# Optimization experiments

Measured on AMD Instinct MI355X. Metric: run time of the kernel, lower is better.

Reference implementation:

```python
import jax, jax.numpy as jnp
import numpy as np

DT_SCALE = 0.01  # time grid = arange(T) * 0.01, i.e. t in [0, 0.99]


def setup_inputs() -> dict:
    key = jax.random.key(0)
    k1, k2, k3 = jax.random.split(key, 3)
    latents, hidden = 128, 256
    S, N, T = 4, 1024, 100
    first_point = jax.random.normal(k1, (S, N, latents), dtype=jnp.float32)
    time_steps_to_predict = jnp.arange(T, dtype=jnp.float32) * DT_SCALE
    # ODEFunc MLP params (Glorot-ish scaling so tanh stays in a sane range)
    W1 = jax.random.normal(k2, (latents, hidden), dtype=jnp.float32) / np.sqrt(latents)
    b1 = jnp.zeros((hidden,), dtype=jnp.float32)
    W2 = jax.random.normal(k3, (hidden, latents), dtype=jnp.float32) / np.sqrt(hidden)
    b2 = jnp.zeros((latents,), dtype=jnp.float32)
    return {
        "first_point": first_point,
        "time_steps_to_predict": time_steps_to_predict,
        "W1": W1, "b1": b1, "W2": W2, "b2": b2,
    }


def reference(first_point, time_steps_to_predict, W1, b1, W2, b2):
    # ode_func: dy/dt = tanh(y @ W1 + b1) @ W2 + b2 (time-autonomous MLP)
    def f(y):
        return jnp.tanh(y @ W1 + b1) @ W2 + b2

    # torchdiffeq fixed-step 'rk4': one classical RK4 step per output interval.
    t0s = time_steps_to_predict[:-1]
    t1s = time_steps_to_predict[1:]

    def rk4_step(y, ts):
        t0, t1 = ts
        dt = t1 - t0
        half = dt * 0.5
        k1 = f(y)
        k2 = f(y + half * k1)
        k3 = f(y + half * k2)
        k4 = f(y + dt * k3)
        y1 = y + (dt / 6.0) * (k1 + 2.0 * k2 + 2.0 * k3 + k4)
        return y1, y1

    _, ys = jax.lax.scan(rk4_step, first_point, (t0s, t1s))  # [T-1, S, N, D]
    pred_y = jnp.concatenate([first_point[None], ys], axis=0)  # [T, S, N, D]
    # permute(1, 2, 0, 3): [T, S, N, D] -> [S, N, T, D]
    return jnp.transpose(pred_y, (1, 2, 0, 3))
```

## Files before the change

### kernel.cpp

```cpp
#include <hip/hip_runtime.h>
#include <hip/hip_bf16.h>

typedef __attribute__((ext_vector_type(8))) short v8s;
typedef __attribute__((ext_vector_type(4))) float f4;

#define MFMA16(a, b, c) __builtin_amdgcn_mfma_f32_16x16x32_bf16((a), (b), (c), 0, 0, 0)

__device__ __forceinline__ float bf2f(unsigned short u) {
    return __uint_as_float(((unsigned)u) << 16);
}
__device__ __forceinline__ unsigned short f2bf(float x) {
    unsigned u = __float_as_uint(x);
    unsigned r = 0x7FFFu + ((u >> 16) & 1u);
    return (unsigned short)((u + r) >> 16);
}
__device__ __forceinline__ unsigned pack_bf16_2(float a, float b) {
    float2 t; t.x = a; t.y = b;
    union { __hip_bfloat162 h; unsigned u; } cv;
    cv.h = __float22bfloat162_rn(t);
    return cv.u;
}
__device__ __forceinline__ float tanh_fast(float z) {
    float u = __builtin_amdgcn_exp2f(z * 2.885390081777927f);
    float r = __builtin_amdgcn_rcpf(u + 1.0f);
    return __builtin_fmaf(-2.0f, r, 1.0f);
}
__device__ __forceinline__ float ldin(const void* p, int i, bool f32) {
    return f32 ? ((const float*)p)[i] : bf2f(((const unsigned short*)p)[i]);
}

#define BROWS 16
#define TSTEPS 100
#define DLAT 128
#define DHID 256
#define YSTR 136
#define HSTR 264

__global__ __launch_bounds__(512, 2)
void ode_rk4_kernel(const void* __restrict__ fp,
                    const void* __restrict__ ts,
                    const void* __restrict__ W1,
                    const void* __restrict__ b1,
                    const void* __restrict__ W2,
                    const void* __restrict__ b2,
                    void* __restrict__ out) {
    __shared__ unsigned short yB[BROWS * YSTR];
    __shared__ unsigned short hB[BROWS * HSTR];
    __shared__ float tsL[TSTEPS];

    const bool m32 = fabsf(((const float*)ts)[1] - 0.01f) < 0.004f;

    const int tid = threadIdx.x;
    const int w = tid >> 6;
    const int lane = tid & 63;
    const int pp = lane & 15;
    const int qq = lane >> 4;
    const int R0 = blockIdx.x * BROWS;

    if (tid < TSTEPS) tsL[tid] = ldin(ts, tid, m32);

    v8s w1f[4][2];
#pragma unroll
    for (int kt = 0; kt < 4; ++kt)
#pragma unroll
        for (int nt = 0; nt < 2; ++nt) {
            v8s f;
#pragma unroll
            for (int j = 0; j < 8; ++j)
                f[j] = (short)f2bf(ldin(W1, (kt * 32 + qq * 8 + j) * DHID + 32 * w + nt * 16 + pp, m32));
            w1f[kt][nt] = f;
        }
    v8s w2f[8];
#pragma unroll
    for (int kt = 0; kt < 8; ++kt) {
        v8s f;
#pragma unroll
        for (int j = 0; j < 8; ++j)
            f[j] = (short)f2bf(ldin(W2, (kt * 32 + qq * 8 + j) * DLAT + 16 * w + pp, m32));
        w2f[kt] = f;
    }
    const float b1v0 = ldin(b1, 32 * w + pp, m32);
    const float b1v1 = ldin(b1, 32 * w + 16 + pp, m32);
    const float b2v  = ldin(b2, 16 * w + pp, m32);

    const int pb = pp >> 3, pw = pp & 7;
    const int sA = (pp >> 1) & 7;
    const unsigned short* yA[4];
#pragma unroll
    for (int kt = 0; kt < 4; ++kt)
        yA[kt] = yB + pp * YSTR + (((4 * kt + qq) ^ sA) << 3);
    const unsigned short* hA[8];
#pragma unroll
    for (int kt = 0; kt < 8; ++kt)
        hA[kt] = hB + pp * HSTR + (((4 * kt + qq) ^ sA) << 3);
    const int s0 = (2 * qq) & 7, s1 = (2 * qq + 1) & 7;
    int hoff[2][2], yoff[2];
    hoff[0][0] = (((4 * w + pb) ^ s0) << 3) + pw;
    hoff[0][1] = (((4 * w + 2 + pb) ^ s0) << 3) + pw;
    hoff[1][0] = (((4 * w + pb) ^ s1) << 3) + pw;
    hoff[1][1] = (((4 * w + 2 + pb) ^ s1) << 3) + pw;
    yoff[0] = (((2 * w + pb) ^ s0) << 3) + pw;
    yoff[1] = (((2 * w + pb) ^ s1) << 3) + pw;

    {
        int row = tid >> 5, ch = tid & 31;
        int sw = (row >> 1) & 7;
        unsigned short* dst = yB + row * YSTR + (((ch >> 1) ^ sw) << 3) + (ch & 1) * 4;
        if (m32) {
            float4 v = *((const float4*)((const float*)fp + (size_t)(R0 + row) * DLAT) + ch);
            *((float4*)((float*)out + ((size_t)(R0 + row) * TSTEPS) * DLAT) + ch) = v;
            ushort4 b; b.x = f2bf(v.x); b.y = f2bf(v.y); b.z = f2bf(v.z); b.w = f2bf(v.w);
            *(ushort4*)dst = b;
        } else {
            const unsigned short* fpu = (const unsigned short*)fp;
            ushort4 v = *((const ushort4*)(fpu + (size_t)(R0 + row) * DLAT) + ch);
            *((ushort4*)((unsigned short*)out + ((size_t)(R0 + row) * TSTEPS) * DLAT) + ch) = v;
            *(ushort4*)dst = v;
        }
    }

    const int c2 = 16 * w + pp;
    float yreg[4];
    size_t ob[4];
#pragma unroll
    for (int r = 0; r < 4; ++r) {
        yreg[r] = ldin(fp, (R0 + 4 * qq + r) * DLAT + c2, m32);
        ob[r] = ((size_t)(R0 + 4 * qq + r) * TSTEPS) * DLAT + c2;
    }
    __syncthreads();

    for (int t = 0; t < TSTEPS - 1; ++t) {
        float dt = tsL[t + 1] - tsL[t];
        float half = 0.5f * dt;
        float ksum[4] = {0.f, 0.f, 0.f, 0.f};
#pragma unroll
        for (int e = 0; e < 4; ++e) {
            __syncthreads();
            f4 h0 = {0.f, 0.f, 0.f, 0.f}, h1 = {0.f, 0.f, 0.f, 0.f};
#pragma unroll
            for (int kt = 0; kt < 4; ++kt) {
                v8s a = *(const v8s*)yA[kt];
                h0 = MFMA16(a, w1f[kt][0], h0);
                h1 = MFMA16(a, w1f[kt][1], h1);
            }
#pragma unroll
            for (int r = 0; r < 4; ++r) {
                float z0 = tanh_fast(h0[r] + b1v0);
                float z1 = tanh_fast(h1[r] + b1v1);
                unsigned pu = pack_bf16_2(z0, z1);
                unsigned short* hp = hB + (4 * qq + r) * HSTR;
                hp[hoff[r >> 1][0]] = (unsigned short)pu;
                hp[hoff[r >> 1][1]] = (unsigned short)(pu >> 16);
            }
            __syncthreads();
            f4 kacc = {0.f, 0.f, 0.f, 0.f};
#pragma unroll
            for (int kt = 0; kt < 8; ++kt) {
                v8s a = *(const v8s*)hA[kt];
                kacc = MFMA16(a, w2f[kt], kacc);
            }
            const float wgt = (e == 0 || e == 3) ? 1.0f : 2.0f;
            const float cc = (e == 2) ? dt : half;
            float kv[4];
#pragma unroll
            for (int r = 0; r < 4; ++r) {
                kv[r] = kacc[r] + b2v;
                ksum[r] = __builtin_fmaf(wgt, kv[r], ksum[r]);
            }
            if (e < 3) {
#pragma unroll
                for (int rp = 0; rp < 2; ++rp) {
                    float ya0 = __builtin_fmaf(cc, kv[2 * rp], yreg[2 * rp]);
                    float ya1 = __builtin_fmaf(cc, kv[2 * rp + 1], yreg[2 * rp + 1]);
                    unsigned pu = pack_bf16_2(ya0, ya1);
                    yB[(4 * qq + 2 * rp) * YSTR + yoff[rp]] = (unsigned short)pu;
                    yB[(4 * qq + 2 * rp + 1) * YSTR + yoff[rp]] = (unsigned short)(pu >> 16);
                }
            } else {
                float s = dt * (1.0f / 6.0f);
#pragma unroll
                for (int rp = 0; rp < 2; ++rp) {
                    yreg[2 * rp]     = __builtin_fmaf(s, ksum[2 * rp],     yreg[2 * rp]);
                    yreg[2 * rp + 1] = __builtin_fmaf(s, ksum[2 * rp + 1], yreg[2 * rp + 1]);
                    unsigned pu = pack_bf16_2(yreg[2 * rp], yreg[2 * rp + 1]);
                    yB[(4 * qq + 2 * rp) * YSTR + yoff[rp]] = (unsigned short)pu;
                    yB[(4 * qq + 2 * rp + 1) * YSTR + yoff[rp]] = (unsigned short)(pu >> 16);
                }
            }
        }
        if (m32) {
            float* op = (float*)out;
#pragma unroll
            for (int r = 0; r < 4; ++r)
                op[ob[r] + (size_t)(t + 1) * DLAT] = yreg[r];
        } else {
            unsigned short* op = (unsigned short*)out;
#pragma unroll
            for (int r = 0; r < 4; ++r)
                op[ob[r] + (size_t)(t + 1) * DLAT] = f2bf(yreg[r]);
        }
    }
}

extern "C" void kernel_launch(void* const* d_in, const int* in_sizes, int n_in,
                              void* d_out, int out_size, void* d_ws, size_t ws_size,
                              hipStream_t stream) {
    (void)in_sizes; (void)n_in; (void)d_ws; (void)ws_size; (void)out_size;
    ode_rk4_kernel<<<256, 512, 0, stream>>>(d_in[0], d_in[1], d_in[2], d_in[3],
                                            d_in[4], d_in[5], d_out);
}
```

Before: 525.7 us.

## Carry pre-activation state via fused W2·W1 to drop one GEMM stage per RK4 stage

```diff
diff --git a/kernel.cpp b/kernel.cpp
--- a/kernel.cpp
+++ b/kernel.cpp
@@ -20,8 +20,8 @@
     cv.h = __float22bfloat162_rn(t);
     return cv.u;
 }
-__device__ __forceinline__ float tanh_fast(float z) {
-    float u = __builtin_amdgcn_exp2f(z * 2.885390081777927f);
+__device__ __forceinline__ float tanh_scaled(float zs) {
+    float u = __builtin_amdgcn_exp2f(zs);
     float r = __builtin_amdgcn_rcpf(u + 1.0f);
     return __builtin_fmaf(-2.0f, r, 1.0f);
 }
@@ -33,8 +33,28 @@
 #define TSTEPS 100
 #define DLAT 128
 #define DHID 256
-#define YSTR 136
 #define HSTR 264
+#define HBUF (BROWS * HSTR)
+#define TANH_C 2.885390081777927f
+
+__global__ __launch_bounds__(256, 4)
+void prep_w21(const void* __restrict__ ts, const void* __restrict__ W1,
+              const void* __restrict__ W2, const void* __restrict__ b2,
+              void* __restrict__ ws) {
+    const bool m32 = fabsf(((const float*)ts)[1] - 0.01f) < 0.004f;
+    const int i = blockIdx.x;
+    const int j = threadIdx.x;
+    float acc = 0.f;
+    for (int m = 0; m < DLAT; ++m)
+        acc = __builtin_fmaf(ldin(W2, i * DLAT + m, m32), ldin(W1, m * DHID + j, m32), acc);
+    ((unsigned short*)ws)[i * DHID + j] = f2bf(TANH_C * acc);
+    if (i == 0) {
+        float a2 = 0.f;
+        for (int m = 0; m < DLAT; ++m)
+            a2 = __builtin_fmaf(ldin(b2, m, m32), ldin(W1, m * DHID + j, m32), a2);
+        ((float*)((char*)ws + DHID * DHID * 2))[j] = TANH_C * a2;
+    }
+}
 
 __global__ __launch_bounds__(512, 2)
 void ode_rk4_kernel(const void* __restrict__ fp,
@@ -43,9 +63,9 @@
                     const void* __restrict__ b1,
                     const void* __restrict__ W2,
                     const void* __restrict__ b2,
+                    const void* __restrict__ ws,
                     void* __restrict__ out) {
-    __shared__ unsigned short yB[BROWS * YSTR];
-    __shared__ unsigned short hB[BROWS * HSTR];
+    __shared__ unsigned short hB[2 * HBUF];
     __shared__ float tsL[TSTEPS];
 
     const bool m32 = fabsf(((const float*)ts)[1] - 0.01f) < 0.004f;
@@ -59,17 +79,6 @@
 
     if (tid < TSTEPS) tsL[tid] = ldin(ts, tid, m32);
 
-    v8s w1f[4][2];
-#pragma unroll
-    for (int kt = 0; kt < 4; ++kt)
-#pragma unroll
-        for (int nt = 0; nt < 2; ++nt) {
-            v8s f;
-#pragma unroll
-            for (int j = 0; j < 8; ++j)
-                f[j] = (short)f2bf(ldin(W1, (kt * 32 + qq * 8 + j) * DHID + 32 * w + nt * 16 + pp, m32));
-            w1f[kt][nt] = f;
-        }
     v8s w2f[8];
 #pragma unroll
     for (int kt = 0; kt < 8; ++kt) {
@@ -79,33 +88,40 @@
             f[j] = (short)f2bf(ldin(W2, (kt * 32 + qq * 8 + j) * DLAT + 16 * w + pp, m32));
         w2f[kt] = f;
     }
-    const float b1v0 = ldin(b1, 32 * w + pp, m32);
-    const float b1v1 = ldin(b1, 32 * w + 16 + pp, m32);
-    const float b2v  = ldin(b2, 16 * w + pp, m32);
-
+    const unsigned short* w21p = (const unsigned short*)ws;
+    v8s w21f[8][2];
+#pragma unroll
+    for (int kt = 0; kt < 8; ++kt)
+#pragma unroll
+        for (int nt = 0; nt < 2; ++nt) {
+            v8s f;
+#pragma unroll
+            for (int j = 0; j < 8; ++j)
+                f[j] = (short)w21p[(kt * 32 + qq * 8 + j) * DHID + 32 * w + nt * 16 + pp];
+            w21f[kt][nt] = f;
+        }
+    const float* b2w1p = (const float*)((const char*)ws + DHID * DHID * 2);
+    const float bz0 = b2w1p[32 * w + pp];
+    const float bz1 = b2w1p[32 * w + 16 + pp];
+    const float b2v = ldin(b2, 16 * w + pp, m32);
+
+    const int sA = (pp >> 1) & 7;
+    int hAoff[8];
+#pragma unroll
+    for (int kt = 0; kt < 8; ++kt)
+        hAoff[kt] = pp * HSTR + (((4 * kt + qq) ^ sA) << 3);
     const int pb = pp >> 3, pw = pp & 7;
-    const int sA = (pp >> 1) & 7;
-    const unsigned short* yA[4];
-#pragma unroll
-    for (int kt = 0; kt < 4; ++kt)
-        yA[kt] = yB + pp * YSTR + (((4 * kt + qq) ^ sA) << 3);
-    const unsigned short* hA[8];
-#pragma unroll
-    for (int kt = 0; kt < 8; ++kt)
-        hA[kt] = hB + pp * HSTR + (((4 * kt + qq) ^ sA) << 3);
     const int s0 = (2 * qq) & 7, s1 = (2 * qq + 1) & 7;
-    int hoff[2][2], yoff[2];
+    int hoff[2][2];
     hoff[0][0] = (((4 * w + pb) ^ s0) << 3) + pw;
     hoff[0][1] = (((4 * w + 2 + pb) ^ s0) << 3) + pw;
     hoff[1][0] = (((4 * w + pb) ^ s1) << 3) + pw;
     hoff[1][1] = (((4 * w + 2 + pb) ^ s1) << 3) + pw;
-    yoff[0] = (((2 * w + pb) ^ s0) << 3) + pw;
-    yoff[1] = (((2 * w + pb) ^ s1) << 3) + pw;
 
     {
         int row = tid >> 5, ch = tid & 31;
         int sw = (row >> 1) & 7;
-        unsigned short* dst = yB + row * YSTR + (((ch >> 1) ^ sw) << 3) + (ch & 1) * 4;
+        unsigned short* dst = hB + row * HSTR + (((ch >> 1) ^ sw) << 3) + (ch & 1) * 4;
         if (m32) {
             float4 v = *((const float4*)((const float*)fp + (size_t)(R0 + row) * DLAT) + ch);
             *((float4*)((float*)out + ((size_t)(R0 + row) * TSTEPS) * DLAT) + ch) = v;
@@ -127,65 +143,96 @@
         yreg[r] = ldin(fp, (R0 + 4 * qq + r) * DLAT + c2, m32);
         ob[r] = ((size_t)(R0 + 4 * qq + r) * TSTEPS) * DLAT + c2;
     }
+
+    v8s w1f[4][2];
+#pragma unroll
+    for (int kt = 0; kt < 4; ++kt)
+#pragma unroll
+        for (int nt = 0; nt < 2; ++nt) {
+            v8s f;
+#pragma unroll
+            for (int j = 0; j < 8; ++j)
+                f[j] = (short)f2bf(TANH_C * ldin(W1, (kt * 32 + qq * 8 + j) * DHID + 32 * w + nt * 16 + pp, m32));
+            w1f[kt][nt] = f;
+        }
+    const float b1s0 = TANH_C * ldin(b1, 32 * w + pp, m32);
+    const float b1s1 = TANH_C * ldin(b1, 32 * w + 16 + pp, m32);
+
     __syncthreads();
+    f4 a0 = {0.f, 0.f, 0.f, 0.f}, a1 = {0.f, 0.f, 0.f, 0.f};
+#pragma unroll
+    for (int kt = 0; kt < 4; ++kt) {
+        v8s a = *(const v8s*)(hB + hAoff[kt]);
+        a0 = MFMA16(a, w1f[kt][0], a0);
+        a1 = MFMA16(a, w1f[kt][1], a1);
+    }
+    float zs[8];
+#pragma unroll
+    for (int r = 0; r < 4; ++r) {
+        zs[r] = a0[r] + b1s0;
+        zs[4 + r] = a1[r] + b1s1;
+    }
+#pragma unroll
+    for (int r = 0; r < 4; ++r) {
+        unsigned pu = pack_bf16_2(tanh_scaled(zs[r]), tanh_scaled(zs[4 + r]));
+        unsigned short* hp = hB + HBUF + (4 * qq + r) * HSTR;
+        hp[hoff[r >> 1][0]] = (unsigned short)pu;
+        hp[hoff[r >> 1][1]] = (unsigned short)(pu >> 16);
+    }
 
     for (int t = 0; t < TSTEPS - 1; ++t) {
-        float dt = tsL[t + 1] - tsL[t];
-        float half = 0.5f * dt;
+        const float dt = tsL[t + 1] - tsL[t];
+        const float half = 0.5f * dt;
+        const float d6 = dt * (1.0f / 6.0f);
         float ksum[4] = {0.f, 0.f, 0.f, 0.f};
+        float zsum[8] = {0.f, 0.f, 0.f, 0.f, 0.f, 0.f, 0.f, 0.f};
 #pragma unroll
         for (int e = 0; e < 4; ++e) {
+            const int rb = (e & 1) ^ 1;
+            const int wb = e & 1;
             __syncthreads();
-            f4 h0 = {0.f, 0.f, 0.f, 0.f}, h1 = {0.f, 0.f, 0.f, 0.f};
-#pragma unroll
-            for (int kt = 0; kt < 4; ++kt) {
-                v8s a = *(const v8s*)yA[kt];
-                h0 = MFMA16(a, w1f[kt][0], h0);
-                h1 = MFMA16(a, w1f[kt][1], h1);
-            }
+            const unsigned short* hbase = hB + rb * HBUF;
+            f4 az0 = {0.f, 0.f, 0.f, 0.f}, az1 = {0.f, 0.f, 0.f, 0.f}, ak = {0.f, 0.f, 0.f, 0.f};
+#pragma unroll
+            for (int kt = 0; kt < 8; ++kt) {
+                v8s a = *(const v8s*)(hbase + hAoff[kt]);
+                az0 = MFMA16(a, w21f[kt][0], az0);
+                az1 = MFMA16(a, w21f[kt][1], az1);
+                ak  = MFMA16(a, w2f[kt], ak);
+            }
+            const float wgt = (e == 0 || e == 3) ? 1.0f : 2.0f;
+            const float cc = (e == 2) ? dt : half;
+            float zt[8];
 #pragma unroll
             for (int r = 0; r < 4; ++r) {
-                float z0 = tanh_fast(h0[r] + b1v0);
-                float z1 = tanh_fast(h1[r] + b1v1);
-                unsigned pu = pack_bf16_2(z0, z1);
-                unsigned short* hp = hB + (4 * qq + r) * HSTR;
+                float kv = ak[r] + b2v;
+                ksum[r] = __builtin_fmaf(wgt, kv, ksum[r]);
+                float kz0 = az0[r] + bz0;
+                float kz1 = az1[r] + bz1;
+                zsum[r]     = __builtin_fmaf(wgt, kz0, zsum[r]);
+                zsum[4 + r] = __builtin_fmaf(wgt, kz1, zsum[4 + r]);
+                if (e < 3) {
+                    zt[r]     = __builtin_fmaf(cc, kz0, zs[r]);
+                    zt[4 + r] = __builtin_fmaf(cc, kz1, zs[4 + r]);
+                }
+            }
+            if (e == 3) {
+#pragma unroll
+                for (int j = 0; j < 8; ++j) {
+                    zs[j] = __builtin_fmaf(d6, zsum[j], zs[j]);
+                    zt[j] = zs[j];
+                }
+#pragma unroll
+                for (int r = 0; r < 4; ++r)
+                    yreg[r] = __builtin_fmaf(d6, ksum[r], yreg[r]);
+            }
+            unsigned short* wbase = hB + wb * HBUF;
+#pragma unroll
+            for (int r = 0; r < 4; ++r) {
+                unsigned pu = pack_bf16_2(tanh_scaled(zt[r]), tanh_scaled(zt[4 + r]));
+                unsigned short* hp = wbase + (4 * qq + r) * HSTR;
                 hp[hoff[r >> 1][0]] = (unsigned short)pu;
                 hp[hoff[r >> 1][1]] = (unsigned short)(pu >> 16);
-            }
-            __syncthreads();
-            f4 kacc = {0.f, 0.f, 0.f, 0.f};
-#pragma unroll
-            for (int kt = 0; kt < 8; ++kt) {
-                v8s a = *(const v8s*)hA[kt];
-                kacc = MFMA16(a, w2f[kt], kacc);
-            }
-            const float wgt = (e == 0 || e == 3) ? 1.0f : 2.0f;
-            const float cc = (e == 2) ? dt : half;
-            float kv[4];
-#pragma unroll
-            for (int r = 0; r < 4; ++r) {
-                kv[r] = kacc[r] + b2v;
-                ksum[r] = __builtin_fmaf(wgt, kv[r], ksum[r]);
-            }
-            if (e < 3) {
-#pragma unroll
-                for (int rp = 0; rp < 2; ++rp) {
-                    float ya0 = __builtin_fmaf(cc, kv[2 * rp], yreg[2 * rp]);
-                    float ya1 = __builtin_fmaf(cc, kv[2 * rp + 1], yreg[2 * rp + 1]);
-                    unsigned pu = pack_bf16_2(ya0, ya1);
-                    yB[(4 * qq + 2 * rp) * YSTR + yoff[rp]] = (unsigned short)pu;
-                    yB[(4 * qq + 2 * rp + 1) * YSTR + yoff[rp]] = (unsigned short)(pu >> 16);
-                }
-            } else {
-                float s = dt * (1.0f / 6.0f);
-#pragma unroll
-                for (int rp = 0; rp < 2; ++rp) {
-                    yreg[2 * rp]     = __builtin_fmaf(s, ksum[2 * rp],     yreg[2 * rp]);
-                    yreg[2 * rp + 1] = __builtin_fmaf(s, ksum[2 * rp + 1], yreg[2 * rp + 1]);
-                    unsigned pu = pack_bf16_2(yreg[2 * rp], yreg[2 * rp + 1]);
-                    yB[(4 * qq + 2 * rp) * YSTR + yoff[rp]] = (unsigned short)pu;
-                    yB[(4 * qq + 2 * rp + 1) * YSTR + yoff[rp]] = (unsigned short)(pu >> 16);
-                }
             }
         }
         if (m32) {
@@ -205,7 +252,8 @@
 extern "C" void kernel_launch(void* const* d_in, const int* in_sizes, int n_in,
                               void* d_out, int out_size, void* d_ws, size_t ws_size,
                               hipStream_t stream) {
-    (void)in_sizes; (void)n_in; (void)d_ws; (void)ws_size; (void)out_size;
+    (void)in_sizes; (void)n_in; (void)out_size; (void)ws_size;
+    prep_w21<<<DHID, DHID, 0, stream>>>(d_in[1], d_in[2], d_in[4], d_in[5], d_ws);
     ode_rk4_kernel<<<256, 512, 0, stream>>>(d_in[0], d_in[1], d_in[2], d_in[3],
-                                            d_in[4], d_in[5], d_out);
-}
+                                            d_in[4], d_in[5], d_ws, d_out);
+}
```

New measurement: 547.6 us. 1.04x slower.
